# Kernel tuning notes

Measured on AMD Instinct MI355X. Metric: run time of the kernel, lower is better.

Reference implementation:

```python
import jax, jax.numpy as jnp
import numpy as np
import math

B, S, H, NH, HD, RD, INNER, MAXPOS, EPS = 2, 2048, 4096, 16, 256, 64, 16384, 2048, 1e-5


def setup_inputs() -> dict:
    key = jax.random.key(0)
    ks = jax.random.split(key, 8)
    sd = 0.02
    return {
        "hidden_states": jax.random.normal(ks[0], (B, S, H), jnp.float32),
        "attention_mask": jnp.ones((B, S), jnp.int32),
        "position_ids": jnp.broadcast_to(jnp.arange(S, dtype=jnp.int32), (B, S)),
        "ln_scale": jnp.ones((H,), jnp.float32),
        "ln_bias": jnp.zeros((H,), jnp.float32),
        "wq": jax.random.normal(ks[1], (H, H), jnp.float32) * sd,
        "wk": jax.random.normal(ks[2], (H, H), jnp.float32) * sd,
        "wv": jax.random.normal(ks[3], (H, H), jnp.float32) * sd,
        "wo": jax.random.normal(ks[4], (H, H), jnp.float32) * sd,
        "w_in": jax.random.normal(ks[5], (H, INNER), jnp.float32) * sd,
        "b_in": jnp.zeros((INNER,), jnp.float32),
        "w_out": jax.random.normal(ks[6], (INNER, H), jnp.float32) * sd,
        "b_out": jnp.zeros((H,), jnp.float32),
    }


def _rotate_every_two(t):
    # interleave (-odd, even) pairs along last dim
    r = jnp.stack((-t[..., 1::2], t[..., ::2]), axis=-1)
    return r.reshape(t.shape)


def reference(hidden_states, attention_mask, position_ids, ln_scale, ln_bias,
              wq, wk, wv, wo, w_in, b_in, w_out, b_out):
    x = hidden_states
    # LayerNorm (single ln feeds both attn and mlp in GPT-J parallel block)
    mu = jnp.mean(x, axis=-1, keepdims=True)
    var = jnp.mean(jnp.square(x - mu), axis=-1, keepdims=True)
    h = (x - mu) * jax.lax.rsqrt(var + EPS) * ln_scale + ln_bias

    # QKV projections (no bias), split heads: [B,S,NH,HD]
    q = (h @ wq).reshape(B, S, NH, HD)
    k = (h @ wk).reshape(B, S, NH, HD)
    v = (h @ wv).reshape(B, S, NH, HD)

    # sinusoidal table over rotary_dim, gathered by position_ids
    pos = jnp.arange(MAXPOS, dtype=jnp.float32)
    inv_freq = 1.0 / (10000.0 ** (jnp.arange(0, RD, 2, dtype=jnp.float32) / RD))
    freqs = pos[:, None] * inv_freq[None, :]          # [MAXPOS, RD//2]
    table = jnp.concatenate([jnp.sin(freqs), jnp.cos(freqs)], axis=-1)  # [MAXPOS, RD]
    sincos = table[position_ids]                      # [B,S,RD]
    sin, cos = jnp.split(sincos, 2, axis=-1)          # each [B,S,RD//2]
    sinr = jnp.repeat(sin[:, :, None, :], 2, axis=3)  # [B,S,1,RD]
    cosr = jnp.repeat(cos[:, :, None, :], 2, axis=3)

    def rope(t):
        return t * cosr + _rotate_every_two(t) * sinr

    q = jnp.concatenate([rope(q[..., :RD]), q[..., RD:]], axis=-1)
    k = jnp.concatenate([rope(k[..., :RD]), k[..., RD:]], axis=-1)

    # combined causal + padding mask -> additive bias
    causal = jnp.tril(jnp.ones((S, S), dtype=bool))
    mask = (attention_mask[:, None, None, :] > 0) & causal[None, None, :, :]
    bias = jnp.where(mask, 0.0, jnp.finfo(jnp.float32).min)  # [B,1,S,S]

    scale = 1.0 / math.sqrt(HD)
    scores = jnp.einsum('bqhd,bkhd->bhqk', q, k) * scale + bias
    attn = jax.nn.softmax(scores, axis=-1)
    ctx = jnp.einsum('bhqk,bkhd->bqhd', attn, v).reshape(B, S, H)
    attn_out = ctx @ wo

    # MLP on the same LN output (parallel residual), gelu_new ~ tanh gelu
    mlp = jax.nn.gelu(h @ w_in + b_in, approximate=True) @ w_out + b_out

    return x + attn_out + mlp
```

## Files before the change

### kernel.cpp

```cpp
#include <hip/hip_runtime.h>
#include <hip/hip_bf16.h>
#include <math.h>

namespace {

constexpr int kB = 2;
constexpr int kS = 2048;
constexpr int kH = 4096;
constexpr int kNH = 16;
constexpr int kHD = 256;

typedef __attribute__((ext_vector_type(4))) float f32x4;
typedef __attribute__((ext_vector_type(8))) short bf16x8;

__device__ __forceinline__ unsigned short f2bf(float f) {
  unsigned int u = __float_as_uint(f);
  u += 0x7FFFu + ((u >> 16) & 1u);
  return (unsigned short)(u >> 16);
}
__device__ __forceinline__ float bf2f(unsigned short h) {
  return __uint_as_float(((unsigned int)h) << 16);
}
__device__ __forceinline__ void gl2lds16(const void* g, void* l) {
  __builtin_amdgcn_global_load_lds(
      (const __attribute__((address_space(1))) unsigned int*)g,
      (__attribute__((address_space(3))) unsigned int*)l, 16, 0, 0);
}

__global__ __launch_bounds__(256) void ln_fwd(
    const float* __restrict__ x, const float* __restrict__ gam,
    const float* __restrict__ bet, unsigned short* __restrict__ hout,
    float* __restrict__ outp) {
  int row = blockIdx.x;
  int t = threadIdx.x;
  const float4* xr = (const float4*)(x + (size_t)row * kH);
  float4 v[4];
  float sum = 0.f, sq = 0.f;
#pragma unroll
  for (int i = 0; i < 4; i++) {
    v[i] = xr[t + i * 256];
    sum += v[i].x + v[i].y + v[i].z + v[i].w;
    sq += v[i].x * v[i].x + v[i].y * v[i].y + v[i].z * v[i].z + v[i].w * v[i].w;
  }
#pragma unroll
  for (int o = 32; o > 0; o >>= 1) {
    sum += __shfl_xor(sum, o);
    sq += __shfl_xor(sq, o);
  }
  __shared__ float red[8];
  if ((t & 63) == 0) { red[t >> 6] = sum; red[4 + (t >> 6)] = sq; }
  __syncthreads();
  sum = red[0] + red[1] + red[2] + red[3];
  sq = red[4] + red[5] + red[6] + red[7];
  float mu = sum * (1.f / kH);
  float rstd = rsqrtf(sq * (1.f / kH) - mu * mu + 1e-5f);
  const float4* gp = (const float4*)gam;
  const float4* bp = (const float4*)bet;
  ushort4* hr = (ushort4*)(hout + (size_t)row * kH);
  float4* orow = (float4*)(outp + (size_t)row * kH);
#pragma unroll
  for (int i = 0; i < 4; i++) {
    float4 g = gp[t + i * 256];
    float4 bb = bp[t + i * 256];
    ushort4 hv;
    hv.x = f2bf((v[i].x - mu) * rstd * g.x + bb.x);
    hv.y = f2bf((v[i].y - mu) * rstd * g.y + bb.y);
    hv.z = f2bf((v[i].z - mu) * rstd * g.z + bb.z);
    hv.w = f2bf((v[i].w - mu) * rstd * g.w + bb.w);
    hr[t + i * 256] = hv;
    orow[t + i * 256] = v[i];
  }
}

__global__ __launch_bounds__(256) void cvt_t(
    const float* __restrict__ in, int ldin, unsigned short* __restrict__ outp,
    int ldout) {
  __shared__ float tile[32][33];
  int n0 = blockIdx.x * 32, k0 = blockIdx.y * 32;
  int tx = threadIdx.x, ty = threadIdx.y;
#pragma unroll
  for (int i = 0; i < 4; i++)
    tile[ty + i * 8][tx] = in[(size_t)(k0 + ty + i * 8) * ldin + n0 + tx];
  __syncthreads();
#pragma unroll
  for (int i = 0; i < 4; i++)
    outp[(size_t)(n0 + ty + i * 8) * ldout + k0 + tx] =
        f2bf(tile[tx][ty + i * 8]);
}

__global__ __launch_bounds__(256) void vtrans(
    const unsigned short* __restrict__ v, unsigned short* __restrict__ vt) {
  __shared__ unsigned short tile[32][33];
  int bh = blockIdx.z;
  int s0 = blockIdx.x * 32, d0 = blockIdx.y * 32;
  int tx = threadIdx.x, ty = threadIdx.y;
  int b = bh >> 4, h = bh & 15;
  const unsigned short* src = v + (size_t)(b * kS) * kH + h * kHD;
#pragma unroll
  for (int i = 0; i < 4; i++)
    tile[ty + i * 8][tx] = src[(size_t)(s0 + ty + i * 8) * kH + d0 + tx];
  __syncthreads();
  unsigned short* dst = vt + (size_t)bh * kHD * kS;
#pragma unroll
  for (int i = 0; i < 4; i++)
    dst[(size_t)(d0 + ty + i * 8) * kS + s0 + tx] = tile[tx][ty + i * 8];
}

__global__ __launch_bounds__(256) void rope_scale(
    unsigned short* __restrict__ q, unsigned short* __restrict__ k,
    const int* __restrict__ pos) {
  int idx = blockIdx.x * 256 + threadIdx.x;
  int j = idx & 127;
  int rowh = idx >> 7;
  int h = rowh & 15;
  int s = (rowh >> 4) & 2047;
  int b = rowh >> 15;
  size_t off = ((size_t)(b * kS + s)) * kH + h * kHD + 2 * j;
  const float SCALE = 0.0625f;
  if (j < 32) {
    int p = pos[b * kS + s];
    float inv = exp2f(-(float)j * (13.287712379549449f / 32.f));
    float fr = (float)p * inv;
    float sn, cs;
    sincosf(fr, &sn, &cs);
    float e = bf2f(q[off]), o = bf2f(q[off + 1]);
    q[off] = f2bf((e * cs - o * sn) * SCALE);
    q[off + 1] = f2bf((o * cs + e * sn) * SCALE);
    e = bf2f(k[off]); o = bf2f(k[off + 1]);
    k[off] = f2bf(e * cs - o * sn);
    k[off + 1] = f2bf(o * cs + e * sn);
  } else {
    q[off] = f2bf(bf2f(q[off]) * SCALE);
    q[off + 1] = f2bf(bf2f(q[off + 1]) * SCALE);
  }
}

#define AF_MMA(P)                                                           \
  {                                                                         \
    bf16x8 af_[2][2];                                                       \
    _Pragma("unroll") for (int fm = 0; fm < 2; fm++)                        \
        _Pragma("unroll") for (int kk = 0; kk < 2; kk++) {                  \
      int q_ = (2 * (P) + fm) * 16 + l15;                                   \
      af_[fm][kk] = *(const bf16x8*)(cur + ((q_ & 64) << 8) + wm * 8192 +   \
                                     ((q_ & 63) << 7) +                     \
                                     ((((kk << 2) | l4) ^ key) << 4));      \
    }                                                                       \
    asm volatile("s_barrier" ::: "memory");                                 \
    __builtin_amdgcn_s_setprio(1);                                          \
    _Pragma("unroll") for (int fm = 0; fm < 2; fm++)                        \
        _Pragma("unroll") for (int fn = 0; fn < 4; fn++)                    \
            _Pragma("unroll") for (int kk = 0; kk < 2; kk++)                \
      acc[2 * (P) + fm][fn] = __builtin_amdgcn_mfma_f32_16x16x32_bf16(      \
          af_[fm][kk], bfr[fn][kk], acc[2 * (P) + fm][fn], 0, 0, 0);        \
    __builtin_amdgcn_s_setprio(0);                                          \
  }

template <int EPI>
__global__ __launch_bounds__(512, 2) void gemm256(
    const unsigned short* __restrict__ A, int lda,
    const unsigned short* __restrict__ Bt, int ldb, void* __restrict__ Cp,
    int ldc, const float* __restrict__ bias, int K, int gx) {
  __shared__ __align__(16) char lds[131072];
  const int t = threadIdx.x;
  const int lane = t & 63, w = t >> 6;
  const int wm = w >> 2, wn = w & 3;
  const int l15 = lane & 15, l4 = lane >> 4;
  const int key = l15 & 7;

  const int nwg = gridDim.x;
  const int orig = blockIdx.x;
  const int wg = (orig & 7) * (nwg >> 3) + (orig >> 3);
  const int bx = wg % gx, by = wg / gx;
  const int m0 = by * 256, n0 = bx * 256;

  const int lr = t >> 3, ch = t & 7;
  const int swk = (ch ^ (lr & 7)) * 8;
  const unsigned short* aE0 = A + (size_t)(m0 + lr) * lda + swk;
  const unsigned short* aE1 = A + (size_t)(m0 + 128 + lr) * lda + swk;
  const unsigned short* aL0 = A + (size_t)(m0 + 64 + lr) * lda + swk;
  const unsigned short* aL1 = A + (size_t)(m0 + 192 + lr) * lda + swk;
  const unsigned short* b00 = Bt + (size_t)(n0 + lr) * ldb + swk;
  const unsigned short* b01 = Bt + (size_t)(n0 + 64 + lr) * ldb + swk;
  const unsigned short* b10 = Bt + (size_t)(n0 + 128 + lr) * ldb + swk;
  const unsigned short* b11 = Bt + (size_t)(n0 + 192 + lr) * ldb + swk;
  const int t16 = t * 16;

  f32x4 acc[8][4];
#pragma unroll
  for (int m = 0; m < 8; m++)
#pragma unroll
    for (int n = 0; n < 4; n++) acc[m][n] = (f32x4)(0.f);

  {
    char* b = lds;
    gl2lds16(b00, b + 32768 + t16); b00 += 64;
    gl2lds16(b01, b + 40960 + t16); b01 += 64;
    gl2lds16(b10, b + 49152 + t16); b10 += 64;
    gl2lds16(b11, b + 57344 + t16); b11 += 64;
    gl2lds16(aE0, b + t16);         aE0 += 64;
    gl2lds16(aE1, b + 8192 + t16);  aE1 += 64;
    gl2lds16(aL0, b + 16384 + t16); aL0 += 64;
    gl2lds16(aL1, b + 24576 + t16); aL1 += 64;
  }
  asm volatile("s_waitcnt vmcnt(0)" ::: "memory");
  asm volatile("s_barrier" ::: "memory");

  const int nt = K >> 6;
  for (int kt = 0; kt < nt; ++kt) {
    const char* cur = lds + (kt & 1) * 65536;
    char* nxt = lds + (((kt & 1) ^ 1)) * 65536;
    const bool pre = (kt + 1 < nt);
    bf16x8 bfr[4][2];
    if (pre) {
      gl2lds16(b00, nxt + 32768 + t16); b00 += 64;
      gl2lds16(b01, nxt + 40960 + t16); b01 += 64;
    }
#pragma unroll
    for (int fn = 0; fn < 4; fn++)
#pragma unroll
      for (int kk = 0; kk < 2; kk++) {
        int n = wn * 64 + fn * 16 + l15;
        bfr[fn][kk] = *(const bf16x8*)(cur + 32768 + (n << 7) +
                                       ((((kk << 2) | l4) ^ key) << 4));
      }
    AF_MMA(0)
    asm volatile("s_barrier" ::: "memory");
    if (pre) {
      gl2lds16(b10, nxt + 49152 + t16); b10 += 64;
      gl2lds16(b11, nxt + 57344 + t16); b11 += 64;
    }
    AF_MMA(1)
    if (pre) asm volatile("s_waitcnt vmcnt(4)" ::: "memory");
    else     asm volatile("s_waitcnt vmcnt(0)" ::: "memory");
    asm volatile("s_barrier" ::: "memory");
    if (pre) {
      gl2lds16(aE0, nxt + t16);        aE0 += 64;
      gl2lds16(aE1, nxt + 8192 + t16); aE1 += 64;
    }
    AF_MMA(2)
    asm volatile("s_barrier" ::: "memory");
    if (pre) {
      gl2lds16(aL0, nxt + 16384 + t16); aL0 += 64;
      gl2lds16(aL1, nxt + 24576 + t16); aL1 += 64;
    }
    AF_MMA(3)
    asm volatile("s_waitcnt lgkmcnt(0)" ::: "memory");
    if (pre) asm volatile("s_waitcnt vmcnt(2)" ::: "memory");
    asm volatile("s_barrier" ::: "memory");
  }

  const int crow = m0 + wm * 128 + l4 * 4;
  const int ccol = n0 + wn * 64 + l15;
#pragma unroll
  for (int m = 0; m < 8; m++) {
#pragma unroll
    for (int n = 0; n < 4; n++) {
      int col = ccol + n * 16;
#pragma unroll
      for (int r = 0; r < 4; r++) {
        int row = crow + m * 16 + r;
        float v = acc[m][n][r];
        size_t idx = (size_t)row * ldc + col;
        if constexpr (EPI == 0) {
          ((unsigned short*)Cp)[idx] = f2bf(v);
        } else if constexpr (EPI == 1) {
          float u = v + bias[col];
          float c = 0.7978845608028654f * (u + 0.044715f * u * u * u);
          float g = u / (1.0f + __expf(-2.0f * c));
          ((unsigned short*)Cp)[idx] = f2bf(g);
        } else if constexpr (EPI == 2) {
          ((float*)Cp)[idx] += v;
        } else {
          ((float*)Cp)[idx] += v + bias[col];
        }
      }
    }
  }
}

__global__ __launch_bounds__(512) void attn_fwd(
    const unsigned short* __restrict__ q, const unsigned short* __restrict__ k,
    const unsigned short* __restrict__ vt, const int* __restrict__ amask,
    unsigned short* __restrict__ ctx) {
  __shared__ __align__(16) char alds[147456];
  const int t = threadIdx.x, lane = t & 63, w = t >> 6;
  const int bid = blockIdx.x;
  const int qb = 15 - (bid >> 5);
  const int bh = bid & 31;
  const int b = bh >> 4, h = bh & 15;
  const int l15 = lane & 15, l4 = lane >> 4;
  const int qbase = qb * 128;

  bf16x8 qf[8];
  {
    int qrow = qbase + w * 16 + l15;
    const unsigned short* qp =
        q + (size_t)(b * kS + qrow) * kH + h * kHD + l4 * 8;
#pragma unroll
    for (int ks = 0; ks < 8; ks++) qf[ks] = *(const bf16x8*)(qp + ks * 32);
  }
  f32x4 o[16];
#pragma unroll
  for (int nf = 0; nf < 16; nf++) o[nf] = (f32x4)(0.f);
  float mr[4] = {-INFINITY, -INFINITY, -INFINITY, -INFINITY};
  float lr[4] = {0.f, 0.f, 0.f, 0.f};

  const unsigned short* kbase = k + (size_t)(b * kS) * kH + h * kHD;
  const unsigned short* vbase = vt + (size_t)bh * kHD * kS;
  unsigned short* sPw = (unsigned short*)(alds + 131072 + w * 2048);
  const int nt = 2 * qb + 2;

  const int krow = t >> 5, kch = t & 31;
  const int kcs = (kch ^ (krow & 7)) * 8;
  const int vrow = t >> 3, vch = t & 7;
  const int vcs = (vch ^ (vrow & 7)) * 8;
  const int t16b = t * 16;

#define ATTN_STAGE(KV0, BUF)                                                 \
  {                                                                          \
    char* kd = alds + (BUF) * 32768;                                         \
    char* vd = alds + 65536 + (BUF) * 32768;                                 \
    _Pragma("unroll") for (int i = 0; i < 4; i++) {                          \
      gl2lds16(kbase + (size_t)((KV0) + krow + i * 16) * kH + kcs,           \
               kd + i * 8192 + t16b);                                        \
      gl2lds16(vbase + (size_t)(vrow + i * 64) * kS + (KV0) + vcs,           \
               vd + i * 8192 + t16b);                                        \
    }                                                                        \
  }

  ATTN_STAGE(0, 0)

  for (int kvt = 0; kvt < nt; kvt++) {
    const int kv0 = kvt * 64;
    const int cb = kvt & 1;
    if (kvt + 1 < nt) {
      ATTN_STAGE(kv0 + 64, cb ^ 1)
      asm volatile("s_waitcnt vmcnt(8)" ::: "memory");
    } else {
      asm volatile("s_waitcnt vmcnt(0)" ::: "memory");
    }
    asm volatile("s_barrier" ::: "memory");

    const unsigned short* sK = (const unsigned short*)(alds + cb * 32768);
    const unsigned short* sV =
        (const unsigned short*)(alds + 65536 + cb * 32768);

    f32x4 sc[4];
#pragma unroll
    for (int g = 0; g < 4; g++) sc[g] = (f32x4)(0.f);
    __builtin_amdgcn_s_setprio(1);
#pragma unroll
    for (int g = 0; g < 4; g++) {
      int row = g * 16 + l15;
#pragma unroll
      for (int ks = 0; ks < 8; ks++) {
        bf16x8 kf =
            *(const bf16x8*)&sK[row * 256 + (((ks * 4 + l4) ^ (row & 7)) * 8)];
        sc[g] = __builtin_amdgcn_mfma_f32_16x16x32_bf16(qf[ks], kf, sc[g], 0, 0, 0);
      }
    }
    __builtin_amdgcn_s_setprio(0);

    int am[4];
#pragma unroll
    for (int g = 0; g < 4; g++) am[g] = amask[b * kS + kv0 + g * 16 + l15];
    float mx[4];
#pragma unroll
    for (int r = 0; r < 4; r++) {
      int qi = qbase + w * 16 + l4 * 4 + r;
      float a = -INFINITY;
#pragma unroll
      for (int g = 0; g < 4; g++) {
        bool ok = (kv0 + g * 16 + l15 <= qi) && (am[g] != 0);
        float s = ok ? sc[g][r] : -INFINITY;
        sc[g][r] = s;
        a = fmaxf(a, s);
      }
#pragma unroll
      for (int d = 1; d < 16; d <<= 1) a = fmaxf(a, __shfl_xor(a, d));
      mx[r] = a;
    }
    bool nd = false;
#pragma unroll
    for (int r = 0; r < 4; r++) nd |= (mx[r] > mr[r] + 8.f);
    if (__any(nd)) {
#pragma unroll
      for (int r = 0; r < 4; r++) {
        float nm = fmaxf(mr[r], mx[r]);
        float c = __expf(mr[r] - nm);
        lr[r] *= c;
        mr[r] = nm;
#pragma unroll
        for (int nf = 0; nf < 16; nf++) o[nf][r] *= c;
      }
    }
#pragma unroll
    for (int r = 0; r < 4; r++) {
      int prow = l4 * 4 + r;
      int pkey = (prow ^ (prow >> 2)) & 7;
      float rs = 0.f;
#pragma unroll
      for (int g = 0; g < 4; g++) {
        float p = __expf(sc[g][r] - mr[r]);
        rs += p;
        int kvl = g * 16 + l15;
        sPw[prow * 64 + (((kvl >> 3) ^ pkey) << 3) + (kvl & 7)] = f2bf(p);
      }
#pragma unroll
      for (int d = 1; d < 16; d <<= 1) rs += __shfl_xor(rs, d);
      lr[r] += rs;
    }
    asm volatile("s_waitcnt lgkmcnt(0)" ::: "memory");

    int rkey = (l15 ^ (l15 >> 2)) & 7;
    bf16x8 pa[2];
#pragma unroll
    for (int ks2 = 0; ks2 < 2; ks2++)
      pa[ks2] = *(const bf16x8*)&sPw[l15 * 64 + (((ks2 * 4 + l4) ^ rkey) << 3)];
    __builtin_amdgcn_s_setprio(1);
#pragma unroll
    for (int nf = 0; nf < 16; nf++) {
      int vr = nf * 16 + l15;
#pragma unroll
      for (int ks2 = 0; ks2 < 2; ks2++) {
        bf16x8 vf =
            *(const bf16x8*)&sV[vr * 64 + (((ks2 * 4 + l4) ^ (vr & 7)) * 8)];
        o[nf] = __builtin_amdgcn_mfma_f32_16x16x32_bf16(pa[ks2], vf, o[nf], 0, 0, 0);
      }
    }
    __builtin_amdgcn_s_setprio(0);
    asm volatile("s_barrier" ::: "memory");
  }

  float invl[4];
#pragma unroll
  for (int r = 0; r < 4; r++) invl[r] = 1.0f / lr[r];
#pragma unroll
  for (int nf = 0; nf < 16; nf++) {
    int d = nf * 16 + l15;
#pragma unroll
    for (int r = 0; r < 4; r++) {
      int qi = qbase + w * 16 + l4 * 4 + r;
      ctx[(size_t)(b * kS + qi) * kH + h * kHD + d] = f2bf(o[nf][r] * invl[r]);
    }
  }
#undef ATTN_STAGE
}

}

extern "C" void kernel_launch(void* const* d_in, const int* in_sizes, int n_in,
                              void* d_out, int out_size, void* d_ws,
                              size_t ws_size, hipStream_t stream) {
  const float* x = (const float*)d_in[0];
  const int* amask = (const int*)d_in[1];
  const int* pos = (const int*)d_in[2];
  const float* lns = (const float*)d_in[3];
  const float* lnb = (const float*)d_in[4];
  const float* wq = (const float*)d_in[5];
  const float* wk = (const float*)d_in[6];
  const float* wv = (const float*)d_in[7];
  const float* wo = (const float*)d_in[8];
  const float* w_in = (const float*)d_in[9];
  const float* b_in = (const float*)d_in[10];
  const float* w_out = (const float*)d_in[11];
  const float* b_out = (const float*)d_in[12];
  float* out = (float*)d_out;

  if (ws_size < 268435456ull) return;
  char* ws = (char*)d_ws;
  unsigned short* h_bf = (unsigned short*)ws;
  unsigned short* big = (unsigned short*)(ws + 33554432ull);
  unsigned short* vbuf = (unsigned short*)(ws + 167772160ull);
  unsigned short* wbuf = (unsigned short*)(ws + 201326592ull);
  unsigned short* mid = big;
  unsigned short* qbuf = big;
  unsigned short* kbuf = big + 16777216;
  unsigned short* vtb = big + 33554432;
  unsigned short* ctxb = vbuf;

  dim3 t256(256);
  dim3 t512(512);
  dim3 t32x8(32, 8);

  ln_fwd<<<kB * kS, t256, 0, stream>>>(x, lns, lnb, h_bf, out);

  for (int c = 0; c < 2; c++) {
    cvt_t<<<dim3(256, 128), t32x8, 0, stream>>>(w_in + c * 8192, 16384, wbuf, 4096);
    gemm256<1><<<dim3(512), t512, 0, stream>>>(
        h_bf, 4096, wbuf, 4096, mid + c * 8192, 16384, b_in + c * 8192, 4096, 32);
  }
  for (int c = 0; c < 2; c++) {
    cvt_t<<<dim3(128, 256), t32x8, 0, stream>>>(
        w_out + (size_t)c * 8192 * 4096, 4096, wbuf, 8192);
    if (c == 0)
      gemm256<3><<<dim3(256), t512, 0, stream>>>(mid + c * 8192, 16384, wbuf,
                                                 8192, out, 4096, b_out, 8192, 16);
    else
      gemm256<2><<<dim3(256), t512, 0, stream>>>(
          mid + c * 8192, 16384, wbuf, 8192, out, 4096, nullptr, 8192, 16);
  }

  const float* wqkv[3] = {wq, wk, wv};
  unsigned short* qkvp[3] = {qbuf, kbuf, vbuf};
  for (int i = 0; i < 3; i++) {
    cvt_t<<<dim3(128, 128), t32x8, 0, stream>>>(wqkv[i], 4096, wbuf, 4096);
    gemm256<0><<<dim3(256), t512, 0, stream>>>(h_bf, 4096, wbuf, 4096,
                                               qkvp[i], 4096, nullptr, 4096, 16);
  }
  rope_scale<<<32768, t256, 0, stream>>>(qbuf, kbuf, pos);
  vtrans<<<dim3(64, 8, 32), t32x8, 0, stream>>>(vbuf, vtb);
  attn_fwd<<<dim3(512), t512, 0, stream>>>(qbuf, kbuf, vtb, amask, ctxb);
  cvt_t<<<dim3(128, 128), t32x8, 0, stream>>>(wo, 4096, wbuf, 4096);
  gemm256<2><<<dim3(256), t512, 0, stream>>>(ctxb, 4096, wbuf, 4096, out,
                                             4096, nullptr, 4096, 16);
}
```

Baseline: 2.080 ms.

## Prefetch B tiles two k-steps ahead in GEMM main loop with split read/MMA phases

Restructures the GEMM k-loop pipeline. The prologue now fills both LDS buffers. B tiles are prefetched two iterations ahead into the current buffer once its B fragments have been read into registers, while A tiles are prefetched one iteration ahead. The A-fragment reads and the MFMA blocks are split into separate macros, with extra barriers and lgkmcnt waits between them. The goal is to hide more global-load latency behind compute. The cost is more barriers per iteration and more complex vmcnt bookkeeping, which risks ordering mistakes.

```diff
diff --git a/kernel.cpp b/kernel.cpp
--- a/kernel.cpp
+++ b/kernel.cpp
@@ -135,25 +135,26 @@
   }
 }
 
-#define AF_MMA(P)                                                           \
-  {                                                                         \
-    bf16x8 af_[2][2];                                                       \
+#define AF_READ(P)                                                          \
     _Pragma("unroll") for (int fm = 0; fm < 2; fm++)                        \
         _Pragma("unroll") for (int kk = 0; kk < 2; kk++) {                  \
       int q_ = (2 * (P) + fm) * 16 + l15;                                   \
       af_[fm][kk] = *(const bf16x8*)(cur + ((q_ & 64) << 8) + wm * 8192 +   \
                                      ((q_ & 63) << 7) +                     \
                                      ((((kk << 2) | l4) ^ key) << 4));      \
-    }                                                                       \
-    asm volatile("s_barrier" ::: "memory");                                 \
+    }
+
+#define DO_MMA(P)                                                           \
     __builtin_amdgcn_s_setprio(1);                                          \
     _Pragma("unroll") for (int fm = 0; fm < 2; fm++)                        \
         _Pragma("unroll") for (int fn = 0; fn < 4; fn++)                    \
             _Pragma("unroll") for (int kk = 0; kk < 2; kk++)                \
       acc[2 * (P) + fm][fn] = __builtin_amdgcn_mfma_f32_16x16x32_bf16(      \
           af_[fm][kk], bfr[fn][kk], acc[2 * (P) + fm][fn], 0, 0, 0);        \
-    __builtin_amdgcn_s_setprio(0);                                          \
-  }
+    __builtin_amdgcn_s_setprio(0);
+
+#define SBAR asm volatile("s_barrier" ::: "memory")
+#define LGKM0 asm volatile("s_waitcnt lgkmcnt(0)" ::: "memory")
 
 template <int EPI>
 __global__ __launch_bounds__(512, 2) void gemm256(
@@ -192,29 +193,37 @@
     for (int n = 0; n < 4; n++) acc[m][n] = (f32x4)(0.f);
 
   {
-    char* b = lds;
-    gl2lds16(b00, b + 32768 + t16); b00 += 64;
-    gl2lds16(b01, b + 40960 + t16); b01 += 64;
-    gl2lds16(b10, b + 49152 + t16); b10 += 64;
-    gl2lds16(b11, b + 57344 + t16); b11 += 64;
-    gl2lds16(aE0, b + t16);         aE0 += 64;
-    gl2lds16(aE1, b + 8192 + t16);  aE1 += 64;
-    gl2lds16(aL0, b + 16384 + t16); aL0 += 64;
-    gl2lds16(aL1, b + 24576 + t16); aL1 += 64;
-  }
-  asm volatile("s_waitcnt vmcnt(0)" ::: "memory");
-  asm volatile("s_barrier" ::: "memory");
+    char* b0 = lds;
+    char* b1 = lds + 65536;
+    gl2lds16(b00, b0 + 32768 + t16); b00 += 64;
+    gl2lds16(b01, b0 + 40960 + t16); b01 += 64;
+    gl2lds16(b10, b0 + 49152 + t16); b10 += 64;
+    gl2lds16(b11, b0 + 57344 + t16); b11 += 64;
+    gl2lds16(aE0, b0 + t16);         aE0 += 64;
+    gl2lds16(aE1, b0 + 8192 + t16);  aE1 += 64;
+    gl2lds16(aL0, b0 + 16384 + t16); aL0 += 64;
+    gl2lds16(aL1, b0 + 24576 + t16); aL1 += 64;
+    gl2lds16(b00, b1 + 32768 + t16); b00 += 64;
+    gl2lds16(b01, b1 + 40960 + t16); b01 += 64;
+    gl2lds16(b10, b1 + 49152 + t16); b10 += 64;
+    gl2lds16(b11, b1 + 57344 + t16); b11 += 64;
+    gl2lds16(aE0, b1 + t16);         aE0 += 64;
+    gl2lds16(aE1, b1 + 8192 + t16);  aE1 += 64;
+    gl2lds16(aL0, b1 + 16384 + t16); aL0 += 64;
+    gl2lds16(aL1, b1 + 24576 + t16); aL1 += 64;
+  }
+  asm volatile("s_waitcnt vmcnt(10)" ::: "memory");
+  SBAR;
 
   const int nt = K >> 6;
   for (int kt = 0; kt < nt; ++kt) {
-    const char* cur = lds + (kt & 1) * 65536;
+    char* curw = lds + (kt & 1) * 65536;
+    const char* cur = curw;
     char* nxt = lds + (((kt & 1) ^ 1)) * 65536;
-    const bool pre = (kt + 1 < nt);
+    const bool stA = (kt >= 1) && (kt + 1 < nt);
+    const bool stB = (kt + 2 < nt);
     bf16x8 bfr[4][2];
-    if (pre) {
-      gl2lds16(b00, nxt + 32768 + t16); b00 += 64;
-      gl2lds16(b01, nxt + 40960 + t16); b01 += 64;
-    }
+    bf16x8 af_[2][2];
 #pragma unroll
     for (int fn = 0; fn < 4; fn++)
 #pragma unroll
@@ -223,30 +232,42 @@
         bfr[fn][kk] = *(const bf16x8*)(cur + 32768 + (n << 7) +
                                        ((((kk << 2) | l4) ^ key) << 4));
       }
-    AF_MMA(0)
-    asm volatile("s_barrier" ::: "memory");
-    if (pre) {
-      gl2lds16(b10, nxt + 49152 + t16); b10 += 64;
-      gl2lds16(b11, nxt + 57344 + t16); b11 += 64;
-    }
-    AF_MMA(1)
-    if (pre) asm volatile("s_waitcnt vmcnt(4)" ::: "memory");
-    else     asm volatile("s_waitcnt vmcnt(0)" ::: "memory");
-    asm volatile("s_barrier" ::: "memory");
-    if (pre) {
+    AF_READ(0)
+    if (stA) {
       gl2lds16(aE0, nxt + t16);        aE0 += 64;
       gl2lds16(aE1, nxt + 8192 + t16); aE1 += 64;
     }
-    AF_MMA(2)
-    asm volatile("s_barrier" ::: "memory");
-    if (pre) {
+    SBAR; LGKM0;
+    DO_MMA(0)
+    SBAR;
+    AF_READ(1)
+    if (stA) {
       gl2lds16(aL0, nxt + 16384 + t16); aL0 += 64;
       gl2lds16(aL1, nxt + 24576 + t16); aL1 += 64;
     }
-    AF_MMA(3)
-    asm volatile("s_waitcnt lgkmcnt(0)" ::: "memory");
-    if (pre) asm volatile("s_waitcnt vmcnt(2)" ::: "memory");
-    asm volatile("s_barrier" ::: "memory");
+    SBAR; LGKM0;
+    DO_MMA(1)
+    if (kt + 1 < nt) asm volatile("s_waitcnt vmcnt(8)" ::: "memory");
+    else             asm volatile("s_waitcnt vmcnt(0)" ::: "memory");
+    SBAR;
+    AF_READ(2)
+    if (stB) {
+      gl2lds16(b00, curw + 32768 + t16); b00 += 64;
+      gl2lds16(b01, curw + 40960 + t16); b01 += 64;
+    }
+    SBAR; LGKM0;
+    DO_MMA(2)
+    SBAR;
+    AF_READ(3)
+    if (stB) {
+      gl2lds16(b10, curw + 49152 + t16); b10 += 64;
+      gl2lds16(b11, curw + 57344 + t16); b11 += 64;
+    }
+    SBAR; LGKM0;
+    DO_MMA(3)
+    if (kt + 2 < nt)      asm volatile("s_waitcnt vmcnt(6)" ::: "memory");
+    else if (kt + 1 < nt) asm volatile("s_waitcnt vmcnt(2)" ::: "memory");
+    SBAR;
   }
 
   const int crow = m0 + wm * 128 + l4 * 4;
```

Measured after the change: 2.041 ms. About the same (-1.9%).
